# Performance work log

Measured on AMD Instinct MI355X. Metric: run time of the kernel, lower is better.

Reference implementation:

```python
import jax, jax.numpy as jnp
import numpy as np

HID = 128; H = 8; D = HID // H; L = 2; IN = 128; OUT = 32
ND = 20000; NF = 50000; E = 400000
SQRT_D = float(np.sqrt(D))
LN_EPS = 1e-5


def setup_inputs() -> dict:
    key = jax.random.key(0)
    ks = jax.random.split(key, 16)
    s = 1.0 / np.sqrt(HID)
    n = lambda k, sh, sc=1.0: jax.random.normal(k, sh, jnp.float32) * sc
    return dict(
        x_device=n(ks[0], (ND, IN)),
        x_feature=n(ks[1], (NF, IN)),
        e_df_src=jax.random.randint(ks[2], (E,), 0, ND),
        e_df_dst=jax.random.randint(ks[3], (E,), 0, NF),
        e_fd_src=jax.random.randint(ks[4], (E,), 0, NF),
        e_fd_dst=jax.random.randint(ks[5], (E,), 0, ND),
        W_dev_in=n(ks[6], (IN, HID), s), b_dev_in=jnp.zeros((HID,), jnp.float32),
        W_feat_in=n(ks[7], (IN, HID), s), b_feat_in=jnp.zeros((HID,), jnp.float32),
        Wk=n(ks[8], (L, 2, HID, HID), s), bk=jnp.zeros((L, 2, HID), jnp.float32),
        Wq=n(ks[9], (L, 2, HID, HID), s), bq=jnp.zeros((L, 2, HID), jnp.float32),
        Wv=n(ks[10], (L, 2, HID, HID), s), bv=jnp.zeros((L, 2, HID), jnp.float32),
        a_rel=n(ks[11], (L, 2, H, D, D), 1.0 / np.sqrt(D)),
        m_rel=n(ks[12], (L, 2, H, D, D), 1.0 / np.sqrt(D)),
        p_rel=jnp.ones((L, 2, H), jnp.float32),
        Wa=n(ks[13], (L, 2, HID, HID), s), ba=jnp.zeros((L, 2, HID), jnp.float32),
        skip=jnp.ones((L, 2), jnp.float32),
        ln_g=jnp.ones((L, 2, HID), jnp.float32), ln_b=jnp.zeros((L, 2, HID), jnp.float32),
        W_out=n(ks[14], (HID, OUT), s), b_out=jnp.zeros((OUT,), jnp.float32),
    )


def _layer_norm(x, g, b):
    m = x.mean(-1, keepdims=True)
    v = ((x - m) ** 2).mean(-1, keepdims=True)
    return (x - m) * jax.lax.rsqrt(v + LN_EPS) * g + b


def _edge_agg(q_dst, k_src, v_src, a_r, m_r, p_r, src, dst, n_dst):
    # per-edge-type relation transforms of source k/v: [N_src,H,D]
    kt = jnp.einsum('nhd,hde->nhe', k_src, a_r)
    vt = jnp.einsum('nhd,hde->nhe', v_src, m_r)
    # per-edge attention logits [E,H], scaled by relation prior
    logit = (q_dst[dst] * kt[src]).sum(-1) * p_r / SQRT_D
    # segment softmax over incoming edges of each dst node (per edge type)
    mx = jax.ops.segment_max(logit, dst, num_segments=n_dst)
    ex = jnp.exp(logit - mx[dst])
    sm = jax.ops.segment_sum(ex, dst, num_segments=n_dst)
    alpha = ex / (sm[dst] + 1e-16)
    # attention-weighted message scatter-sum -> [n_dst,H,D]
    return jax.ops.segment_sum(vt[src] * alpha[..., None], dst, num_segments=n_dst)


def _forward(x_device, x_feature, W_dev_in, b_dev_in, W_feat_in, b_feat_in,
             Wk, bk, Wq, bq, Wv, bv, a_rel, m_rel, p_rel, Wa, ba, skip,
             ln_g, ln_b, W_out, b_out, e_df_src, e_df_dst, e_fd_src, e_fd_dst):
    x_d = jax.nn.relu(x_device @ W_dev_in + b_dev_in)
    x_f = jax.nn.relu(x_feature @ W_feat_in + b_feat_in)
    for l in range(L):
        xs = (x_d, x_f)  # node-type 0 = device, 1 = feature
        k = [(xs[t] @ Wk[l, t] + bk[l, t]).reshape(-1, H, D) for t in range(2)]
        q = [(xs[t] @ Wq[l, t] + bq[l, t]).reshape(-1, H, D) for t in range(2)]
        v = [(xs[t] @ Wv[l, t] + bv[l, t]).reshape(-1, H, D) for t in range(2)]
        # edge type 0: device -> feature ; edge type 1: feature -> device
        agg_f = _edge_agg(q[1], k[0], v[0], a_rel[l, 0], m_rel[l, 0], p_rel[l, 0],
                          e_df_src, e_df_dst, NF)
        agg_d = _edge_agg(q[0], k[1], v[1], a_rel[l, 1], m_rel[l, 1], p_rel[l, 1],
                          e_fd_src, e_fd_dst, ND)
        new = []
        for t, agg in ((0, agg_d), (1, agg_f)):
            o = jax.nn.gelu(agg.reshape(-1, HID), approximate=False) @ Wa[l, t] + ba[l, t]
            sk = jax.nn.sigmoid(skip[l, t])
            o = sk * o + (1.0 - sk) * xs[t]              # HGTConv skip
            new.append(_layer_norm(xs[t] + o, ln_g[l, t], ln_b[l, t]))  # wrapper residual+LN (dropout=identity in eval)
        x_d, x_f = new
    return x_d @ W_out + b_out


def reference(x_device, x_feature, e_df_src, e_df_dst, e_fd_src, e_fd_dst,
              W_dev_in, b_dev_in, W_feat_in, b_feat_in, Wk, bk, Wq, bq, Wv, bv,
              a_rel, m_rel, p_rel, Wa, ba, skip, ln_g, ln_b, W_out, b_out):
    return _forward(x_device, x_feature, W_dev_in, b_dev_in, W_feat_in, b_feat_in,
                    Wk, bk, Wq, bq, Wv, bv, a_rel, m_rel, p_rel, Wa, ba, skip,
                    ln_g, ln_b, W_out, b_out, e_df_src, e_df_dst, e_fd_src, e_fd_dst)
```

## Files before the change

### kernel.cpp

```cpp
#include <hip/hip_runtime.h>
#include <math.h>

#define ND 20000
#define NF 50000
#define NE 400000
#define NT (NF + ND)
#define NBKT 256
#define BKTW 274

typedef __attribute__((ext_vector_type(8))) short short8;
typedef __attribute__((ext_vector_type(4))) float f32x4;
typedef unsigned short us;

static __device__ __forceinline__ us f2bf(float f) {
    unsigned u = __builtin_bit_cast(unsigned, f);
    u += 0x7FFF + ((u >> 16) & 1);
    return (us)(u >> 16);
}
static __device__ __forceinline__ float bf2f(us h) {
    return __builtin_bit_cast(float, (unsigned)h << 16);
}
static __device__ __forceinline__ float bflo(unsigned u) {
    return __builtin_bit_cast(float, u << 16);
}
static __device__ __forceinline__ float bfhi(unsigned u) {
    return __builtin_bit_cast(float, u & 0xFFFF0000u);
}
static __device__ __forceinline__ float gelu_f(float x) {
    return 0.5f * x * (1.0f + erff(x * 0.70710678118654752f));
}

__global__ void k_hist_prep(const int* __restrict__ dA, const int* __restrict__ dB,
                            int* __restrict__ blockhist, int HB,
                            const float* __restrict__ W_dev_in, const float* __restrict__ W_feat_in,
                            const float* __restrict__ Wq, const float* __restrict__ Wk,
                            const float* __restrict__ Wv, const float* __restrict__ Wa,
                            const float* __restrict__ b_dev_in, const float* __restrict__ b_feat_in,
                            const float* __restrict__ bq, const float* __restrict__ bk,
                            const float* __restrict__ bv, const float* __restrict__ ba,
                            const float* __restrict__ a_rel, const float* __restrict__ m_rel,
                            const float* __restrict__ p_rel,
                            us* __restrict__ WT, float* __restrict__ B_all) {
    __shared__ int hist[NBKT];
    if ((int)blockIdx.x < HB) {
        hist[threadIdx.x] = 0;
        __syncthreads();
        int base_e = blockIdx.x * 4096;
        #pragma unroll
        for (int j = 0; j < 16; ++j) {
            int e = base_e + j * 256 + threadIdx.x;
            if (e < 2 * NE) {
                int g = (e < NE) ? dA[e] : (NF + dB[e - NE]);
                atomicAdd(&hist[g / BKTW], 1);
            }
        }
        __syncthreads();
        blockhist[blockIdx.x * NBKT + threadIdx.x] = hist[threadIdx.x];
        return;
    }
    int idx = (blockIdx.x - HB) * 256 + threadIdx.x;
    if (idx < 18 * 16384) {
        int k = idx & 127, c = (idx >> 7) & 127, id = idx >> 14;
        float val;
        if (id == 0) val = W_dev_in[k * 128 + c];
        else if (id == 1) val = W_feat_in[k * 128 + c];
        else if (id < 6) val = Wq[(id - 2) * 16384 + k * 128 + c];
        else if (id < 10) {
            int lt = id - 6, h = c >> 4, e = c & 15;
            const float* A = a_rel + (lt * 8 + h) * 256;
            const float* Ws = Wk + lt * 16384 + k * 128 + h * 16;
            float sm = 0.f;
            #pragma unroll
            for (int d = 0; d < 16; ++d) sm += Ws[d] * A[d * 16 + e];
            val = sm * p_rel[lt * 8 + h] * 0.25f;
        } else if (id < 14) {
            int lt = id - 10, h = c >> 4, e = c & 15;
            const float* A = m_rel + (lt * 8 + h) * 256;
            const float* Ws = Wv + lt * 16384 + k * 128 + h * 16;
            float sm = 0.f;
            #pragma unroll
            for (int d = 0; d < 16; ++d) sm += Ws[d] * A[d * 16 + e];
            val = sm;
        } else val = Wa[(id - 14) * 16384 + k * 128 + c];
        WT[(size_t)id * 16384 + (((c * 128 + k)) ^ ((c & 7) << 3))] = f2bf(val);
    } else {
        int j = idx - 18 * 16384;
        if (j >= 18 * 128) return;
        int c = j & 127, id = j >> 7;
        float v;
        if (id == 0) v = b_dev_in[c];
        else if (id == 1) v = b_feat_in[c];
        else if (id < 6) v = bq[(id - 2) * 128 + c];
        else if (id < 10) {
            int lt = id - 6, h = c >> 4, e = c & 15;
            const float* A = a_rel + (lt * 8 + h) * 256;
            const float* bs = bk + lt * 128 + h * 16;
            float sm = 0.f;
            #pragma unroll
            for (int d = 0; d < 16; ++d) sm += bs[d] * A[d * 16 + e];
            v = sm * p_rel[lt * 8 + h] * 0.25f;
        } else if (id < 14) {
            int lt = id - 10, h = c >> 4, e = c & 15;
            const float* A = m_rel + (lt * 8 + h) * 256;
            const float* bs = bv + lt * 128 + h * 16;
            float sm = 0.f;
            #pragma unroll
            for (int d = 0; d < 16; ++d) sm += bs[d] * A[d * 16 + e];
            v = sm;
        } else v = ba[(id - 14) * 128 + c];
        B_all[j] = v;
    }
}

__global__ void k_scanA(int* __restrict__ blockhist, int* __restrict__ totals, int HB) {
    __shared__ int sd[256];
    int b = blockIdx.x, t = threadIdx.x;
    int v = (t < HB) ? blockhist[t * NBKT + b] : 0;
    sd[t] = v; __syncthreads();
    for (int off = 1; off < 256; off <<= 1) {
        int add = (t >= off) ? sd[t - off] : 0;
        __syncthreads();
        sd[t] += add;
        __syncthreads();
    }
    if (t < HB) blockhist[t * NBKT + b] = sd[t] - v;
    if (t == 255) totals[b] = sd[255];
}

__global__ void k_scanB(const int* __restrict__ totals, int* __restrict__ base) {
    __shared__ int sd[256];
    int t = threadIdx.x;
    int v = totals[t];
    sd[t] = v; __syncthreads();
    for (int off = 1; off < 256; off <<= 1) {
        int add = (t >= off) ? sd[t - off] : 0;
        __syncthreads();
        sd[t] += add;
        __syncthreads();
    }
    base[t] = sd[t] - v;
    if (t == 255) base[256] = sd[255];
}

__global__ void k_scatter(const int* __restrict__ sA, const int* __restrict__ dA,
                          const int* __restrict__ sB, const int* __restrict__ dB,
                          const int* __restrict__ blockhist, const int* __restrict__ base,
                          uint2* __restrict__ pairs) {
    __shared__ int lcur[NBKT];
    int t = threadIdx.x;
    lcur[t] = base[t] + blockhist[blockIdx.x * NBKT + t];
    __syncthreads();
    int base_e = blockIdx.x * 4096;
    #pragma unroll
    for (int j = 0; j < 16; ++j) {
        int e = base_e + j * 256 + t;
        if (e < 2 * NE) {
            int src, g;
            if (e < NE) { src = sA[e]; g = dA[e]; }
            else        { src = sB[e - NE]; g = NF + dB[e - NE]; }
            int pos = atomicAdd(&lcur[g / BKTW], 1);
            pairs[pos] = make_uint2((unsigned)src, (unsigned)g);
        }
    }
}

__global__ void k_bucket_csr(const uint2* __restrict__ pairs, const int* __restrict__ base,
                             int* __restrict__ rs, int* __restrict__ esrc) {
    __shared__ int cnt[BKTW];
    __shared__ int excl[BKTW];
    int b = blockIdx.x, t = threadIdx.x;
    int start = base[b], end = base[b + 1];
    int g0 = b * BKTW;
    for (int i = t; i < BKTW; i += 256) cnt[i] = 0;
    __syncthreads();
    for (int i = start + t; i < end; i += 256)
        atomicAdd(&cnt[(int)pairs[i].y - g0], 1);
    __syncthreads();
    if (t < 64) {
        int lane = t;
        int vals[5]; int s = 0;
        #pragma unroll
        for (int j = 0; j < 5; ++j) {
            int i = lane * 5 + j;
            vals[j] = (i < BKTW) ? cnt[i] : 0;
            s += vals[j];
        }
        int incl = s;
        #pragma unroll
        for (int off = 1; off < 64; off <<= 1) {
            int n = __shfl_up(incl, off);
            if (lane >= off) incl += n;
        }
        int run = incl - s;
        #pragma unroll
        for (int j = 0; j < 5; ++j) {
            int i = lane * 5 + j;
            if (i < BKTW) excl[i] = run;
            run += vals[j];
        }
    }
    __syncthreads();
    int nloc = min(BKTW, NT - g0);
    for (int i = t; i < nloc; i += 256) rs[g0 + i] = start + excl[i];
    if (b == NBKT - 1 && t == 0) rs[NT] = base[NBKT];
    __syncthreads();
    for (int i = start + t; i < end; i += 256) {
        uint2 p = pairs[i];
        int pos = start + atomicAdd(&excl[(int)p.y - g0], 1);
        esrc[pos] = (int)p.x;
    }
}

template<int MODE, int AF32, int RELU>
__global__ __launch_bounds__(256) void mfma_gemm2(
    const void* __restrict__ X0, const void* __restrict__ X1,
    const us* __restrict__ WT0, const float* __restrict__ Ball,
    us* __restrict__ Y0, us* __restrict__ Y1,
    int N0, int N1, int GB0, int widbase,
    us* __restrict__ K0, us* __restrict__ K1,
    const float* __restrict__ skipv, const float* __restrict__ lng,
    const float* __restrict__ lnb) {
    __shared__ us Wlds[16384];
    const int type = (blockIdx.x >= (unsigned)GB0) ? 1 : 0;
    const int bx = blockIdx.x - (type ? GB0 : 0);
    const int N = type ? N1 : N0;
    const void* Xv = type ? X1 : X0;
    const int wid = widbase + type + 4 * blockIdx.y;
    const us* WT = WT0 + (size_t)wid * 16384;
    const float* bias = Ball + wid * 128;

    const int lane = threadIdx.x & 63;
    const int wave = threadIdx.x >> 6;
    const int row_base = bx * 128 + wave * 32;
    const int l15 = lane & 15, lg = lane >> 4;
    const int kbase = lg * 8;

    {
        const char* gsrc = (const char*)WT + wave * 8192 + lane * 16;
        char* ldst = (char*)Wlds + wave * 8192;
        #pragma unroll
        for (int i = 0; i < 8; ++i) {
            __builtin_amdgcn_global_load_lds(
                (const __attribute__((address_space(1))) void*)(gsrc + i * 1024),
                (__attribute__((address_space(3))) void*)(ldst + i * 1024),
                16, 0, 0);
        }
    }

    short8 a[2][4];
    #pragma unroll
    for (int mf = 0; mf < 2; ++mf) {
        int r = row_base + mf * 16 + l15;
        r = r < N ? r : N - 1;
        if (AF32) {
            const float* Xf = (const float*)Xv + (size_t)r * 128;
            #pragma unroll
            for (int kf = 0; kf < 4; ++kf) {
                float4 lo = *(const float4*)(Xf + kf * 32 + kbase);
                float4 hi = *(const float4*)(Xf + kf * 32 + kbase + 4);
                short8 t;
                t[0] = (short)f2bf(lo.x); t[1] = (short)f2bf(lo.y);
                t[2] = (short)f2bf(lo.z); t[3] = (short)f2bf(lo.w);
                t[4] = (short)f2bf(hi.x); t[5] = (short)f2bf(hi.y);
                t[6] = (short)f2bf(hi.z); t[7] = (short)f2bf(hi.w);
                a[mf][kf] = t;
            }
        } else {
            const us* Xb = (const us*)Xv + (size_t)r * 128;
            #pragma unroll
            for (int kf = 0; kf < 4; ++kf)
                a[mf][kf] = *(const short8*)(Xb + kf * 32 + kbase);
        }
    }

    __syncthreads();

    f32x4 acc[2][8];
    #pragma unroll
    for (int mf = 0; mf < 2; ++mf)
        #pragma unroll
        for (int cf = 0; cf < 8; ++cf) acc[mf][cf] = (f32x4){0.f, 0.f, 0.f, 0.f};

    const unsigned swz = (unsigned)((l15 & 7) << 4);
    #pragma unroll
    for (int cf = 0; cf < 8; ++cf) {
        const unsigned rowbyte = (unsigned)((cf * 16 + l15) * 256 + kbase * 2);
        #pragma unroll
        for (int kf = 0; kf < 4; ++kf) {
            short8 b = *(const short8*)((const char*)Wlds + ((rowbyte + kf * 64) ^ swz));
            acc[0][cf] = __builtin_amdgcn_mfma_f32_16x16x32_bf16(a[0][kf], b, acc[0][cf], 0, 0, 0);
            acc[1][cf] = __builtin_amdgcn_mfma_f32_16x16x32_bf16(a[1][kf], b, acc[1][cf], 0, 0, 0);
        }
    }

    float bval[8];
    #pragma unroll
    for (int cf = 0; cf < 8; ++cf) bval[cf] = bias[cf * 16 + l15];

    if (MODE == 2) {
        const int lt = widbase - 14 + type;
        float sk = 1.f / (1.f + __expf(-skipv[lt]));
        float gv[8], bv2[8];
        #pragma unroll
        for (int cf = 0; cf < 8; ++cf) {
            gv[cf]  = lng[(size_t)lt * 128 + cf * 16 + l15];
            bv2[cf] = lnb[(size_t)lt * 128 + cf * 16 + l15];
        }
        us* xw = type ? K1 : K0;
        #pragma unroll
        for (int mf = 0; mf < 2; ++mf)
            #pragma unroll
            for (int r = 0; r < 4; ++r) {
                int grow = row_base + mf * 16 + lg * 4 + r;
                if (grow >= N) continue;
                float t[8];
                float sum = 0.f;
                #pragma unroll
                for (int cf = 0; cf < 8; ++cf) {
                    float o = acc[mf][cf][r] + bval[cf];
                    float x = bf2f(xw[(size_t)grow * 128 + cf * 16 + l15]);
                    t[cf] = (2.f - sk) * x + sk * o;
                    sum += t[cf];
                }
                sum += __shfl_xor(sum, 1); sum += __shfl_xor(sum, 2);
                sum += __shfl_xor(sum, 4); sum += __shfl_xor(sum, 8);
                float mean = sum * (1.0f / 128.0f);
                float vs = 0.f;
                #pragma unroll
                for (int cf = 0; cf < 8; ++cf) { t[cf] -= mean; vs += t[cf] * t[cf]; }
                vs += __shfl_xor(vs, 1); vs += __shfl_xor(vs, 2);
                vs += __shfl_xor(vs, 4); vs += __shfl_xor(vs, 8);
                float inv = rsqrtf(vs * (1.0f / 128.0f) + 1e-5f);
                #pragma unroll
                for (int cf = 0; cf < 8; ++cf)
                    xw[(size_t)grow * 128 + cf * 16 + l15] = f2bf(t[cf] * inv * gv[cf] + bv2[cf]);
            }
        return;
    }

    #pragma unroll
    for (int mf = 0; mf < 2; ++mf)
        #pragma unroll
        for (int r = 0; r < 4; ++r) {
            int grow = row_base + mf * 16 + lg * 4 + r;
            if (grow >= N) continue;
            #pragma unroll
            for (int cf = 0; cf < 8; ++cf) {
                float v = acc[mf][cf][r] + bval[cf];
                if (RELU) v = fmaxf(v, 0.f);
                us val = f2bf(v);
                int col = cf * 16 + l15;
                if (MODE == 0 || blockIdx.y == 0) {
                    (type ? Y1 : Y0)[(size_t)grow * 128 + col] = val;
                } else {
                    (type ? K1 : K0)[(size_t)grow * 256 + (blockIdx.y - 1) * 128 + col] = val;
                }
            }
        }
}

__global__ __launch_bounds__(256) void gemm_out_k(
    const us* __restrict__ X, const float* __restrict__ W,
    const float* __restrict__ bias, float* __restrict__ Y, int N) {
    __shared__ float Ws[128 * 32];
    __shared__ float Xs[8][128];
    const int tid = threadIdx.x;
    const int row0 = blockIdx.x * 8;
    #pragma unroll
    for (int it = 0; it < 16; ++it) Ws[it * 256 + tid] = W[it * 256 + tid];
    #pragma unroll
    for (int it = 0; it < 2; ++it) {
        int idx = it * 256 + tid;
        int rr = idx >> 6, kp = idx & 63;
        int gr = row0 + rr;
        unsigned u = (gr < N) ? *(const unsigned*)(X + (size_t)gr * 128 + kp * 2) : 0u;
        Xs[rr][kp * 2]     = bflo(u);
        Xs[rr][kp * 2 + 1] = bfhi(u);
    }
    __syncthreads();
    const int rr = tid >> 5, c = tid & 31;
    float acc = bias[c];
    #pragma unroll 8
    for (int k = 0; k < 128; ++k)
        acc = fmaf(Xs[rr][k], Ws[k * 32 + c], acc);
    int gr = row0 + rr;
    if (gr < N) Y[(size_t)gr * 32 + c] = acc;
}

#define EDGE_STEP(kc, vc, pidx)                                        \
    {                                                                  \
        float part = qv[0] * bflo(kc.x);                               \
        part = fmaf(qv[1], bfhi(kc.x), part);                          \
        part = fmaf(qv[2], bflo(kc.y), part);                          \
        part = fmaf(qv[3], bfhi(kc.y), part);                          \
        part = fmaf(qv[4], bflo(kc.z), part);                          \
        part = fmaf(qv[5], bfhi(kc.z), part);                          \
        part = fmaf(qv[6], bflo(kc.w), part);                          \
        part = fmaf(qv[7], bfhi(kc.w), part);                          \
        part += __shfl_xor(part, 1);                                   \
        float w = ((pidx) < p1) ? __expf(part) : 0.f;                  \
        s += w;                                                        \
        a[0] = fmaf(w, bflo(vc.x), a[0]);                              \
        a[1] = fmaf(w, bfhi(vc.x), a[1]);                              \
        a[2] = fmaf(w, bflo(vc.y), a[2]);                              \
        a[3] = fmaf(w, bfhi(vc.y), a[3]);                              \
        a[4] = fmaf(w, bflo(vc.z), a[4]);                              \
        a[5] = fmaf(w, bfhi(vc.z), a[5]);                              \
        a[6] = fmaf(w, bflo(vc.w), a[6]);                              \
        a[7] = fmaf(w, bfhi(vc.w), a[7]);                              \
    }

__global__ __launch_bounds__(256) void edge_agg3(
    const us* __restrict__ q, const us* __restrict__ kv,
    const int* __restrict__ rs, const int* __restrict__ esrc,
    us* __restrict__ agg, int n_dst, int goff) {
    int dst = (blockIdx.x * 256 + threadIdx.x) >> 4;
    int li = threadIdx.x & 15;
    if (dst >= n_dst) return;
    int g = dst + goff;

    uint4 qb = *(const uint4*)(q + (size_t)dst * 128 + li * 8);
    float qv[8];
    qv[0] = bflo(qb.x); qv[1] = bfhi(qb.x);
    qv[2] = bflo(qb.y); qv[3] = bfhi(qb.y);
    qv[4] = bflo(qb.z); qv[5] = bfhi(qb.z);
    qv[6] = bflo(qb.w); qv[7] = bfhi(qb.w);

    const int p0 = rs[g], p1 = rs[g + 1];
    float s = 0.f;
    float a[8];
    #pragma unroll
    for (int j = 0; j < 8; ++j) a[j] = 0.f;

    const size_t loff = (size_t)li * 8;
    uint4 kA0, vA0, kA1, vA1, kB0, vB0, kB1, vB1;
    int sN0, sN1, sN2, sN3;

    if (p0 < p1) {
        const int last = p1 - 1;
        int i0 = p0, i1 = min(p0 + 1, last), i2 = min(p0 + 2, last), i3 = min(p0 + 3, last);
        int s0 = esrc[i0], s1 = esrc[i1], s2 = esrc[i2], s3 = esrc[i3];
        kA0 = *(const uint4*)(kv + (size_t)s0 * 256 + loff);
        vA0 = *(const uint4*)(kv + (size_t)s0 * 256 + 128 + loff);
        kA1 = *(const uint4*)(kv + (size_t)s1 * 256 + loff);
        vA1 = *(const uint4*)(kv + (size_t)s1 * 256 + 128 + loff);
        kB0 = *(const uint4*)(kv + (size_t)s2 * 256 + loff);
        vB0 = *(const uint4*)(kv + (size_t)s2 * 256 + 128 + loff);
        kB1 = *(const uint4*)(kv + (size_t)s3 * 256 + loff);
        vB1 = *(const uint4*)(kv + (size_t)s3 * 256 + 128 + loff);
        sN0 = esrc[min(p0 + 4, last)];
        sN1 = esrc[min(p0 + 5, last)];
        sN2 = esrc[min(p0 + 6, last)];
        sN3 = esrc[min(p0 + 7, last)];

        for (int p = p0; p < p1; p += 4) {
            const int lastc = last;
            EDGE_STEP(kA0, vA0, p);
            EDGE_STEP(kA1, vA1, p + 1);
            kA0 = *(const uint4*)(kv + (size_t)sN0 * 256 + loff);
            vA0 = *(const uint4*)(kv + (size_t)sN0 * 256 + 128 + loff);
            kA1 = *(const uint4*)(kv + (size_t)sN1 * 256 + loff);
            vA1 = *(const uint4*)(kv + (size_t)sN1 * 256 + 128 + loff);
            sN0 = esrc[min(p + 8, lastc)];
            sN1 = esrc[min(p + 9, lastc)];
            EDGE_STEP(kB0, vB0, p + 2);
            EDGE_STEP(kB1, vB1, p + 3);
            kB0 = *(const uint4*)(kv + (size_t)sN2 * 256 + loff);
            vB0 = *(const uint4*)(kv + (size_t)sN2 * 256 + 128 + loff);
            kB1 = *(const uint4*)(kv + (size_t)sN3 * 256 + loff);
            vB1 = *(const uint4*)(kv + (size_t)sN3 * 256 + 128 + loff);
            sN2 = esrc[min(p + 10, lastc)];
            sN3 = esrc[min(p + 11, lastc)];
        }
    }

    float r = 1.0f / (s + 1e-16f);
    unsigned o[4];
    #pragma unroll
    for (int j = 0; j < 4; ++j) {
        us lo = f2bf(gelu_f(a[2 * j] * r));
        us hi = f2bf(gelu_f(a[2 * j + 1] * r));
        o[j] = (unsigned)lo | ((unsigned)hi << 16);
    }
    *(uint4*)(agg + (size_t)dst * 128 + li * 8) = make_uint4(o[0], o[1], o[2], o[3]);
}

extern "C" void kernel_launch(void* const* d_in, const int* in_sizes, int n_in,
                              void* d_out, int out_size, void* d_ws, size_t ws_size,
                              hipStream_t stream) {
    const float* x_device = (const float*)d_in[0];
    const float* x_feature = (const float*)d_in[1];
    const int* e_df_src = (const int*)d_in[2];
    const int* e_df_dst = (const int*)d_in[3];
    const int* e_fd_src = (const int*)d_in[4];
    const int* e_fd_dst = (const int*)d_in[5];
    const float* W_dev_in = (const float*)d_in[6];
    const float* b_dev_in = (const float*)d_in[7];
    const float* W_feat_in = (const float*)d_in[8];
    const float* b_feat_in = (const float*)d_in[9];
    const float* Wk = (const float*)d_in[10];
    const float* bk = (const float*)d_in[11];
    const float* Wq = (const float*)d_in[12];
    const float* bq = (const float*)d_in[13];
    const float* Wv = (const float*)d_in[14];
    const float* bv = (const float*)d_in[15];
    const float* a_rel = (const float*)d_in[16];
    const float* m_rel = (const float*)d_in[17];
    const float* p_rel = (const float*)d_in[18];
    const float* Wa = (const float*)d_in[19];
    const float* ba = (const float*)d_in[20];
    const float* skip = (const float*)d_in[21];
    const float* ln_g = (const float*)d_in[22];
    const float* ln_b = (const float*)d_in[23];
    const float* W_out = (const float*)d_in[24];
    const float* b_out = (const float*)d_in[25];

    char* ws = (char*)d_ws;
    size_t off = 0;
    auto alloc = [&](size_t bytes) -> void* {
        void* p = ws + off;
        off = (off + bytes + 255) & ~(size_t)255;
        return p;
    };
    us* xd     = (us*)alloc((size_t)ND * 128 * 2);
    us* xf     = (us*)alloc((size_t)NF * 128 * 2);
    us* q_d    = (us*)alloc((size_t)ND * 128 * 2);
    us* q_f    = (us*)alloc((size_t)NF * 128 * 2);
    us* kv_d   = (us*)alloc((size_t)ND * 256 * 2);
    us* kv_f   = (us*)alloc((size_t)NF * 256 * 2);
    us* agg_d  = (us*)alloc((size_t)ND * 128 * 2);
    us* agg_f  = (us*)alloc((size_t)NF * 128 * 2);
    us* WT     = (us*)alloc((size_t)18 * 16384 * 2);
    float* B_all = (float*)alloc(18 * 128 * 4);
    int* rs     = (int*)alloc((size_t)(NT + 1) * 4);
    int* esrc   = (int*)alloc((size_t)(2 * NE + 8) * 4);
    uint2* pairs = (uint2*)alloc((size_t)2 * NE * 8);
    int* blockhist = (int*)alloc((size_t)200 * NBKT * 4);
    int* totals = (int*)alloc(NBKT * 4);
    int* base   = (int*)alloc((NBKT + 1) * 4);

    const int HB = (2 * NE + 4095) / 4096;
    const int PB = (18 * 16384 + 18 * 128 + 255) / 256;

    k_hist_prep<<<HB + PB, 256, 0, stream>>>(
        e_df_dst, e_fd_dst, blockhist, HB,
        W_dev_in, W_feat_in, Wq, Wk, Wv, Wa,
        b_dev_in, b_feat_in, bq, bk, bv, ba,
        a_rel, m_rel, p_rel, WT, B_all);
    k_scanA<<<NBKT, 256, 0, stream>>>(blockhist, totals, HB);
    k_scanB<<<1, 256, 0, stream>>>(totals, base);
    k_scatter<<<HB, 256, 0, stream>>>(e_df_src, e_df_dst, e_fd_src, e_fd_dst,
                                      blockhist, base, pairs);
    k_bucket_csr<<<NBKT, 256, 0, stream>>>(pairs, base, rs, esrc);

    const int GBD = (ND + 127) / 128, GBF = (NF + 127) / 128;

    mfma_gemm2<0, 1, 1><<<dim3(GBD + GBF, 1), 256, 0, stream>>>(
        x_device, x_feature, WT, B_all, xd, xf, ND, NF, GBD, 0,
        nullptr, nullptr, nullptr, nullptr, nullptr);

    for (int l = 0; l < 2; ++l) {
        mfma_gemm2<1, 0, 0><<<dim3(GBD + GBF, 3), 256, 0, stream>>>(
            xd, xf, WT, B_all, q_d, q_f, ND, NF, GBD, 2 + l * 2,
            kv_d, kv_f, nullptr, nullptr, nullptr);

        edge_agg3<<<((NF * 16) + 255) / 256, 256, 0, stream>>>(
            q_f, kv_d, rs, esrc, agg_f, NF, 0);
        edge_agg3<<<((ND * 16) + 255) / 256, 256, 0, stream>>>(
            q_d, kv_f, rs, esrc, agg_d, ND, NF);

        mfma_gemm2<2, 0, 0><<<dim3(GBD + GBF, 1), 256, 0, stream>>>(
            agg_d, agg_f, WT, B_all, nullptr, nullptr, ND, NF, GBD, 14 + l * 2,
            xd, xf, skip, ln_g, ln_b);
    }

    gemm_out_k<<<(ND + 7) / 8, 256, 0, stream>>>(xd, W_out, b_out, (float*)d_out, ND);
}
```

Baseline: 272.4 us.

## Sort destination nodes by in-degree and merge edge aggregation launches

Adds a counting sort of all destination nodes by incoming-edge count (histogram, two scans, permutation write) once per call, then runs a single merged edge-aggregation kernel over the degree-sorted permutation covering both node types. The intent is to balance work within wavefronts, since nodes with similar degree share a warp, and to drop one launch per layer. In exchange it adds four small kernels, an indirection through perm, and scattered q/agg accesses that lose the locality of the natural node order.

Result: no change. 268.8 us (-1.3%).

```diff
diff --git a/kernel.cpp b/kernel.cpp
--- a/kernel.cpp
+++ b/kernel.cpp
@@ -7,6 +7,7 @@
 #define NT (NF + ND)
 #define NBKT 256
 #define BKTW 274
+#define DB 18
 
 typedef __attribute__((ext_vector_type(8))) short short8;
 typedef __attribute__((ext_vector_type(4))) float f32x4;
@@ -208,6 +209,65 @@
         uint2 p = pairs[i];
         int pos = start + atomicAdd(&excl[(int)p.y - g0], 1);
         esrc[pos] = (int)p.x;
+    }
+}
+
+__global__ void k_deghist(const int* __restrict__ rs, int* __restrict__ dh) {
+    __shared__ int h[256];
+    int t = threadIdx.x;
+    h[t] = 0;
+    __syncthreads();
+    int base_n = blockIdx.x * 4096;
+    #pragma unroll
+    for (int j = 0; j < 16; ++j) {
+        int g = base_n + j * 256 + t;
+        if (g < NT) atomicAdd(&h[min(rs[g + 1] - rs[g], 255)], 1);
+    }
+    __syncthreads();
+    dh[blockIdx.x * 256 + t] = h[t];
+}
+
+__global__ void k_degscanA(int* __restrict__ dh, int* __restrict__ dtot) {
+    int bin = blockIdx.x, t = threadIdx.x;
+    int v = (t < DB) ? dh[t * 256 + bin] : 0;
+    int incl = v;
+    #pragma unroll
+    for (int off = 1; off < 64; off <<= 1) {
+        int n = __shfl_up(incl, off);
+        if (t >= off) incl += n;
+    }
+    if (t < DB) dh[t * 256 + bin] = incl - v;
+    if (t == 63) dtot[bin] = incl;
+}
+
+__global__ void k_degscanB(const int* __restrict__ dtot, int* __restrict__ dbase) {
+    __shared__ int sd[256];
+    int t = threadIdx.x;
+    int v = dtot[255 - t];
+    sd[t] = v; __syncthreads();
+    for (int off = 1; off < 256; off <<= 1) {
+        int add = (t >= off) ? sd[t - off] : 0;
+        __syncthreads();
+        sd[t] += add;
+        __syncthreads();
+    }
+    dbase[255 - t] = sd[t] - v;
+}
+
+__global__ void k_permwrite(const int* __restrict__ rs, const int* __restrict__ dh,
+                            const int* __restrict__ dbase, int* __restrict__ perm) {
+    __shared__ int cur[256];
+    int t = threadIdx.x;
+    cur[t] = dbase[t] + dh[blockIdx.x * 256 + t];
+    __syncthreads();
+    int base_n = blockIdx.x * 4096;
+    #pragma unroll
+    for (int j = 0; j < 16; ++j) {
+        int g = base_n + j * 256 + t;
+        if (g < NT) {
+            int pos = atomicAdd(&cur[min(rs[g + 1] - rs[g], 255)], 1);
+            perm[pos] = g;
+        }
     }
 }
 
@@ -410,14 +470,19 @@
         a[7] = fmaf(w, bfhi(vc.w), a[7]);                              \
     }
 
-__global__ __launch_bounds__(256) void edge_agg3(
-    const us* __restrict__ q, const us* __restrict__ kv,
+__global__ __launch_bounds__(256) void edge_agg4(
+    const us* __restrict__ qf, const us* __restrict__ qd,
+    const us* __restrict__ kvf, const us* __restrict__ kvd,
     const int* __restrict__ rs, const int* __restrict__ esrc,
-    us* __restrict__ agg, int n_dst, int goff) {
-    int dst = (blockIdx.x * 256 + threadIdx.x) >> 4;
+    const int* __restrict__ perm,
+    us* __restrict__ aggf, us* __restrict__ aggd) {
+    int gi = (blockIdx.x * 256 + threadIdx.x) >> 4;
     int li = threadIdx.x & 15;
-    if (dst >= n_dst) return;
-    int g = dst + goff;
+    if (gi >= NT) return;
+    int g = perm[gi];
+    const us *q, *kv; us* agg; int dst;
+    if (g < NF) { dst = g;      q = qf; kv = kvd; agg = aggf; }
+    else        { dst = g - NF; q = qd; kv = kvf; agg = aggd; }
 
     uint4 qb = *(const uint4*)(q + (size_t)dst * 128 + li * 8);
     float qv[8];
@@ -538,6 +603,10 @@
     int* blockhist = (int*)alloc((size_t)200 * NBKT * 4);
     int* totals = (int*)alloc(NBKT * 4);
     int* base   = (int*)alloc((NBKT + 1) * 4);
+    int* dh     = (int*)alloc((size_t)DB * 256 * 4);
+    int* dtot   = (int*)alloc(256 * 4);
+    int* dbase  = (int*)alloc(256 * 4);
+    int* perm   = (int*)alloc((size_t)NT * 4);
 
     const int HB = (2 * NE + 4095) / 4096;
     const int PB = (18 * 16384 + 18 * 128 + 255) / 256;
@@ -553,6 +622,11 @@
                                       blockhist, base, pairs);
     k_bucket_csr<<<NBKT, 256, 0, stream>>>(pairs, base, rs, esrc);
 
+    k_deghist<<<DB, 256, 0, stream>>>(rs, dh);
+    k_degscanA<<<256, 64, 0, stream>>>(dh, dtot);
+    k_degscanB<<<1, 256, 0, stream>>>(dtot, dbase);
+    k_permwrite<<<DB, 256, 0, stream>>>(rs, dh, dbase, perm);
+
     const int GBD = (ND + 127) / 128, GBF = (NF + 127) / 128;
 
     mfma_gemm2<0, 1, 1><<<dim3(GBD + GBF, 1), 256, 0, stream>>>(
@@ -564,10 +638,8 @@
             xd, xf, WT, B_all, q_d, q_f, ND, NF, GBD, 2 + l * 2,
             kv_d, kv_f, nullptr, nullptr, nullptr);
 
-        edge_agg3<<<((NF * 16) + 255) / 256, 256, 0, stream>>>(
-            q_f, kv_d, rs, esrc, agg_f, NF, 0);
-        edge_agg3<<<((ND * 16) + 255) / 256, 256, 0, stream>>>(
-            q_d, kv_f, rs, esrc, agg_d, ND, NF);
+        edge_agg4<<<((NT * 16) + 255) / 256, 256, 0, stream>>>(
+            q_f, q_d, kv_f, kv_d, rs, esrc, perm, agg_f, agg_d);
 
         mfma_gemm2<2, 0, 0><<<dim3(GBD + GBF, 1), 256, 0, stream>>>(
             agg_d, agg_f, WT, B_all, nullptr, nullptr, ND, NF, GBD, 14 + l * 2,
```

## Reuse loaded activation tile across Q/K/V projections and merge edge aggregation launches

Applied to the files above, without the earlier changes.

The QKV projection GEMM no longer launches a 3-deep grid that reloads the same input rows once per projection. Each block now keeps its A fragments in registers and loops over the three weight matrices, reloading the weight tile into LDS between passes with barriers. The two per-direction edge aggregation kernels are fused into one launch that picks its buffers by global node index, saving a launch and filling the GPU better. The trade-off is fewer, longer blocks with the weight reload serialized inside each block instead of spread across parallel blocks.

Result: no change. 267.7 us (-1.7%).

```diff
diff --git a/kernel.cpp b/kernel.cpp
--- a/kernel.cpp
+++ b/kernel.cpp
@@ -225,9 +225,7 @@
     const int bx = blockIdx.x - (type ? GB0 : 0);
     const int N = type ? N1 : N0;
     const void* Xv = type ? X1 : X0;
-    const int wid = widbase + type + 4 * blockIdx.y;
-    const us* WT = WT0 + (size_t)wid * 16384;
-    const float* bias = Ball + wid * 128;
+    const int NP = (MODE == 1) ? 3 : 1;
 
     const int lane = threadIdx.x & 63;
     const int wave = threadIdx.x >> 6;
@@ -235,13 +233,14 @@
     const int l15 = lane & 15, lg = lane >> 4;
     const int kbase = lg * 8;
 
+    const char* gsrc0 = (const char*)(WT0 + (size_t)(widbase + type) * 16384)
+                        + wave * 8192 + lane * 16;
     {
-        const char* gsrc = (const char*)WT + wave * 8192 + lane * 16;
         char* ldst = (char*)Wlds + wave * 8192;
         #pragma unroll
         for (int i = 0; i < 8; ++i) {
             __builtin_amdgcn_global_load_lds(
-                (const __attribute__((address_space(1))) void*)(gsrc + i * 1024),
+                (const __attribute__((address_space(1))) void*)(gsrc0 + i * 1024),
                 (__attribute__((address_space(3))) void*)(ldst + i * 1024),
                 16, 0, 0);
         }
@@ -275,88 +274,109 @@
 
     __syncthreads();
 
-    f32x4 acc[2][8];
-    #pragma unroll
-    for (int mf = 0; mf < 2; ++mf)
-        #pragma unroll
-        for (int cf = 0; cf < 8; ++cf) acc[mf][cf] = (f32x4){0.f, 0.f, 0.f, 0.f};
-
     const unsigned swz = (unsigned)((l15 & 7) << 4);
-    #pragma unroll
-    for (int cf = 0; cf < 8; ++cf) {
-        const unsigned rowbyte = (unsigned)((cf * 16 + l15) * 256 + kbase * 2);
-        #pragma unroll
-        for (int kf = 0; kf < 4; ++kf) {
-            short8 b = *(const short8*)((const char*)Wlds + ((rowbyte + kf * 64) ^ swz));
-            acc[0][cf] = __builtin_amdgcn_mfma_f32_16x16x32_bf16(a[0][kf], b, acc[0][cf], 0, 0, 0);
-            acc[1][cf] = __builtin_amdgcn_mfma_f32_16x16x32_bf16(a[1][kf], b, acc[1][cf], 0, 0, 0);
-        }
-    }
-
-    float bval[8];
-    #pragma unroll
-    for (int cf = 0; cf < 8; ++cf) bval[cf] = bias[cf * 16 + l15];
-
-    if (MODE == 2) {
-        const int lt = widbase - 14 + type;
-        float sk = 1.f / (1.f + __expf(-skipv[lt]));
-        float gv[8], bv2[8];
+
+    for (int p = 0; p < NP; ++p) {
+        const int wid = widbase + type + 4 * p;
+        const float* bias = Ball + wid * 128;
+
+        f32x4 acc[2][8];
+        #pragma unroll
+        for (int mf = 0; mf < 2; ++mf)
+            #pragma unroll
+            for (int cf = 0; cf < 8; ++cf) acc[mf][cf] = (f32x4){0.f, 0.f, 0.f, 0.f};
+
         #pragma unroll
         for (int cf = 0; cf < 8; ++cf) {
-            gv[cf]  = lng[(size_t)lt * 128 + cf * 16 + l15];
-            bv2[cf] = lnb[(size_t)lt * 128 + cf * 16 + l15];
-        }
-        us* xw = type ? K1 : K0;
-        #pragma unroll
-        for (int mf = 0; mf < 2; ++mf)
-            #pragma unroll
-            for (int r = 0; r < 4; ++r) {
-                int grow = row_base + mf * 16 + lg * 4 + r;
-                if (grow >= N) continue;
-                float t[8];
-                float sum = 0.f;
+            const unsigned rowbyte = (unsigned)((cf * 16 + l15) * 256 + kbase * 2);
+            #pragma unroll
+            for (int kf = 0; kf < 4; ++kf) {
+                short8 b = *(const short8*)((const char*)Wlds + ((rowbyte + kf * 64) ^ swz));
+                acc[0][cf] = __builtin_amdgcn_mfma_f32_16x16x32_bf16(a[0][kf], b, acc[0][cf], 0, 0, 0);
+                acc[1][cf] = __builtin_amdgcn_mfma_f32_16x16x32_bf16(a[1][kf], b, acc[1][cf], 0, 0, 0);
+            }
+        }
+
+        if (MODE == 1 && p + 1 < NP) {
+            __syncthreads();
+            const char* gsrc = (const char*)(WT0 + (size_t)(widbase + type + 4 * (p + 1)) * 16384)
+                               + wave * 8192 + lane * 16;
+            char* ldst = (char*)Wlds + wave * 8192;
+            #pragma unroll
+            for (int i = 0; i < 8; ++i) {
+                __builtin_amdgcn_global_load_lds(
+                    (const __attribute__((address_space(1))) void*)(gsrc + i * 1024),
+                    (__attribute__((address_space(3))) void*)(ldst + i * 1024),
+                    16, 0, 0);
+            }
+        }
+
+        float bval[8];
+        #pragma unroll
+        for (int cf = 0; cf < 8; ++cf) bval[cf] = bias[cf * 16 + l15];
+
+        if (MODE == 2) {
+            const int lt = widbase - 14 + type;
+            float sk = 1.f / (1.f + __expf(-skipv[lt]));
+            float gv[8], bv2[8];
+            #pragma unroll
+            for (int cf = 0; cf < 8; ++cf) {
+                gv[cf]  = lng[(size_t)lt * 128 + cf * 16 + l15];
+                bv2[cf] = lnb[(size_t)lt * 128 + cf * 16 + l15];
+            }
+            us* xw = type ? K1 : K0;
+            #pragma unroll
+            for (int mf = 0; mf < 2; ++mf)
                 #pragma unroll
-                for (int cf = 0; cf < 8; ++cf) {
-                    float o = acc[mf][cf][r] + bval[cf];
-                    float x = bf2f(xw[(size_t)grow * 128 + cf * 16 + l15]);
-                    t[cf] = (2.f - sk) * x + sk * o;
-                    sum += t[cf];
+                for (int r = 0; r < 4; ++r) {
+                    int grow = row_base + mf * 16 + lg * 4 + r;
+                    if (grow >= N) continue;
+                    float t[8];
+                    float sum = 0.f;
+                    #pragma unroll
+                    for (int cf = 0; cf < 8; ++cf) {
+                        float o = acc[mf][cf][r] + bval[cf];
+                        float x = bf2f(xw[(size_t)grow * 128 + cf * 16 + l15]);
+                        t[cf] = (2.f - sk) * x + sk * o;
+                        sum += t[cf];
+                    }
+                    sum += __shfl_xor(sum, 1); sum += __shfl_xor(sum, 2);
+                    sum += __shfl_xor(sum, 4); sum += __shfl_xor(sum, 8);
+                    float mean = sum * (1.0f / 128.0f);
+                    float vs = 0.f;
+                    #pragma unroll
+                    for (int cf = 0; cf < 8; ++cf) { t[cf] -= mean; vs += t[cf] * t[cf]; }
+                    vs += __shfl_xor(vs, 1); vs += __shfl_xor(vs, 2);
+                    vs += __shfl_xor(vs, 4); vs += __shfl_xor(vs, 8);
+                    float inv = rsqrtf(vs * (1.0f / 128.0f) + 1e-5f);
+                    #pragma unroll
+                    for (int cf = 0; cf < 8; ++cf)
+                        xw[(size_t)grow * 128 + cf * 16 + l15] = f2bf(t[cf] * inv * gv[cf] + bv2[cf]);
                 }
-                sum += __shfl_xor(sum, 1); sum += __shfl_xor(sum, 2);
-                sum += __shfl_xor(sum, 4); sum += __shfl_xor(sum, 8);
-                float mean = sum * (1.0f / 128.0f);
-                float vs = 0.f;
+        } else {
+            #pragma unroll
+            for (int mf = 0; mf < 2; ++mf)
                 #pragma unroll
-                for (int cf = 0; cf < 8; ++cf) { t[cf] -= mean; vs += t[cf] * t[cf]; }
-                vs += __shfl_xor(vs, 1); vs += __shfl_xor(vs, 2);
-                vs += __shfl_xor(vs, 4); vs += __shfl_xor(vs, 8);
-                float inv = rsqrtf(vs * (1.0f / 128.0f) + 1e-5f);
-                #pragma unroll
-                for (int cf = 0; cf < 8; ++cf)
-                    xw[(size_t)grow * 128 + cf * 16 + l15] = f2bf(t[cf] * inv * gv[cf] + bv2[cf]);
-            }
-        return;
-    }
-
-    #pragma unroll
-    for (int mf = 0; mf < 2; ++mf)
-        #pragma unroll
-        for (int r = 0; r < 4; ++r) {
-            int grow = row_base + mf * 16 + lg * 4 + r;
-            if (grow >= N) continue;
-            #pragma unroll
-            for (int cf = 0; cf < 8; ++cf) {
-                float v = acc[mf][cf][r] + bval[cf];
-                if (RELU) v = fmaxf(v, 0.f);
-                us val = f2bf(v);
-                int col = cf * 16 + l15;
-                if (MODE == 0 || blockIdx.y == 0) {
-                    (type ? Y1 : Y0)[(size_t)grow * 128 + col] = val;
-                } else {
-                    (type ? K1 : K0)[(size_t)grow * 256 + (blockIdx.y - 1) * 128 + col] = val;
+                for (int r = 0; r < 4; ++r) {
+                    int grow = row_base + mf * 16 + lg * 4 + r;
+                    if (grow >= N) continue;
+                    #pragma unroll
+                    for (int cf = 0; cf < 8; ++cf) {
+                        float v = acc[mf][cf][r] + bval[cf];
+                        if (RELU) v = fmaxf(v, 0.f);
+                        us val = f2bf(v);
+                        int col = cf * 16 + l15;
+                        if (MODE == 0 || p == 0) {
+                            (type ? Y1 : Y0)[(size_t)grow * 128 + col] = val;
+                        } else {
+                            (type ? K1 : K0)[(size_t)grow * 256 + (p - 1) * 128 + col] = val;
+                        }
+                    }
                 }
-            }
-        }
+        }
+
+        if (MODE == 1 && p + 1 < NP) __syncthreads();
+    }
 }
 
 __global__ __launch_bounds__(256) void gemm_out_k(
@@ -410,14 +430,17 @@
         a[7] = fmaf(w, bfhi(vc.w), a[7]);                              \
     }
 
-__global__ __launch_bounds__(256) void edge_agg3(
-    const us* __restrict__ q, const us* __restrict__ kv,
+__global__ __launch_bounds__(256) void edge_agg5(
+    const us* __restrict__ qf, const us* __restrict__ qd,
+    const us* __restrict__ kvf, const us* __restrict__ kvd,
     const int* __restrict__ rs, const int* __restrict__ esrc,
-    us* __restrict__ agg, int n_dst, int goff) {
-    int dst = (blockIdx.x * 256 + threadIdx.x) >> 4;
+    us* __restrict__ aggf, us* __restrict__ aggd) {
+    int g = (blockIdx.x * 256 + threadIdx.x) >> 4;
     int li = threadIdx.x & 15;
-    if (dst >= n_dst) return;
-    int g = dst + goff;
+    if (g >= NT) return;
+    const us *q, *kv; us* agg; int dst;
+    if (g < NF) { dst = g;      q = qf; kv = kvd; agg = aggf; }
+    else        { dst = g - NF; q = qd; kv = kvf; agg = aggd; }
 
     uint4 qb = *(const uint4*)(q + (size_t)dst * 128 + li * 8);
     float qv[8];
@@ -555,21 +578,19 @@
 
     const int GBD = (ND + 127) / 128, GBF = (NF + 127) / 128;
 
-    mfma_gemm2<0, 1, 1><<<dim3(GBD + GBF, 1), 256, 0, stream>>>(
+    mfma_gemm2<0, 1, 1><<<GBD + GBF, 256, 0, stream>>>(
         x_device, x_feature, WT, B_all, xd, xf, ND, NF, GBD, 0,
         nullptr, nullptr, nullptr, nullptr, nullptr);
 
     for (int l = 0; l < 2; ++l) {
-        mfma_gemm2<1, 0, 0><<<dim3(GBD + GBF, 3), 256, 0, stream>>>(
+        mfma_gemm2<1, 0, 0><<<GBD + GBF, 256, 0, stream>>>(
             xd, xf, WT, B_all, q_d, q_f, ND, NF, GBD, 2 + l * 2,
             kv_d, kv_f, nullptr, nullptr, nullptr);
 
-        edge_agg3<<<((NF * 16) + 255) / 256, 256, 0, stream>>>(
-            q_f, kv_d, rs, esrc, agg_f, NF, 0);
-        edge_agg3<<<((ND * 16) + 255) / 256, 256, 0, stream>>>(
-            q_d, kv_f, rs, esrc, agg_d, ND, NF);
-
-        mfma_gemm2<2, 0, 0><<<dim3(GBD + GBF, 1), 256, 0, stream>>>(
+        edge_agg5<<<((NT * 16) + 255) / 256, 256, 0, stream>>>(
+            q_f, q_d, kv_f, kv_d, rs, esrc, agg_f, agg_d);
+
+        mfma_gemm2<2, 0, 0><<<GBD + GBF, 256, 0, stream>>>(
             agg_d, agg_f, WT, B_all, nullptr, nullptr, ND, NF, GBD, 14 + l * 2,
             xd, xf, skip, ln_g, ln_b);
     }
```
